# Optimization experiments

Hardware: AMD Instinct MI355X
Metric: run time of the kernel (lower is better)

Reference implementation:

```python
import jax, jax.numpy as jnp
import numpy as np

N = 50000          # total nodes (1000 graphs x 50 agents)
E = 800000         # edges
B = 1000           # batch of graphs -> one agent node each
IN_DIM = 64
HID = 32           # hidden_dim == TransformerConv out_channels per head
HEADS = 4
OUT_DIM = 5
FINAL = HID + HID * HEADS * 2  # 288


def _tconv(x, src, dst, wq, bq, wk, bk, wv, bv):
    """PyG TransformerConv, root_weight=False, concat=True, no edge_attr."""
    n = x.shape[0]
    q = (x @ wq + bq).reshape(n, HEADS, HID)
    k = (x @ wk + bk).reshape(n, HEADS, HID)
    v = (x @ wv + bv).reshape(n, HEADS, HID)
    # per-edge attention logits: query at target, key at source
    alpha = jnp.sum(q[dst] * k[src], axis=-1) / jnp.sqrt(jnp.float32(HID))  # [E, HEADS]
    # segment softmax over incoming edges of each target node
    amax = jax.lax.stop_gradient(jax.ops.segment_max(alpha, dst, num_segments=n))
    ex = jnp.exp(alpha - amax[dst])
    denom = jax.ops.segment_sum(ex, dst, num_segments=n)
    attn = ex / (denom[dst] + 1e-16)                                        # [E, HEADS]
    out = jax.ops.segment_sum(v[src] * attn[..., None], dst, num_segments=n)
    return out.reshape(n, HEADS * HID)


def setup_inputs() -> dict:
    key = jax.random.key(0)
    ks = jax.random.split(key, 24)
    g = lambda i, shape, fan: (jax.random.normal(ks[i], shape, jnp.float32)
                               / jnp.sqrt(jnp.float32(fan)))
    d1 = HID * HEADS  # conv1 output width / conv2 input width
    inp = {
        "x": jax.random.normal(ks[0], (N, IN_DIM), jnp.float32),
        "edge_index": jax.random.randint(ks[1], (2, E), 0, N, jnp.int64),
        "dm_mask": (jax.random.uniform(ks[2], (N, 1)) > 0.5).astype(jnp.float32),
        "global_indices": jax.random.randint(ks[3], (B,), 0, N, jnp.int64),
        # encoder MLP: in -> hid (relu) -> hid
        "enc_w1": g(4, (IN_DIM, HID), IN_DIM), "enc_b1": jnp.zeros((HID,), jnp.float32),
        "enc_w2": g(5, (HID, HID), HID),       "enc_b2": jnp.zeros((HID,), jnp.float32),
        # conv1: hid -> heads*hid
        "c1_wq": g(6, (HID, d1), HID), "c1_bq": jnp.zeros((d1,), jnp.float32),
        "c1_wk": g(7, (HID, d1), HID), "c1_bk": jnp.zeros((d1,), jnp.float32),
        "c1_wv": g(8, (HID, d1), HID), "c1_bv": jnp.zeros((d1,), jnp.float32),
        # conv2: heads*hid -> heads*hid
        "c2_wq": g(9, (d1, d1), d1),  "c2_bq": jnp.zeros((d1,), jnp.float32),
        "c2_wk": g(10, (d1, d1), d1), "c2_bk": jnp.zeros((d1,), jnp.float32),
        "c2_wv": g(11, (d1, d1), d1), "c2_bv": jnp.zeros((d1,), jnp.float32),
        # output head
        "out_w": g(12, (FINAL, OUT_DIM), FINAL),
        "out_b": jnp.zeros((OUT_DIM,), jnp.float32),
    }
    return inp


def reference(x, edge_index, dm_mask, global_indices,
              enc_w1, enc_b1, enc_w2, enc_b2,
              c1_wq, c1_bq, c1_wk, c1_bk, c1_wv, c1_bv,
              c2_wq, c2_bq, c2_wk, c2_bk, c2_wv, c2_bv,
              out_w, out_b):
    src, dst = edge_index[0], edge_index[1]
    # encoder MLP + relu (forward applies F.relu on encoder output)
    h = jax.nn.relu(x @ enc_w1 + enc_b1)
    h = jax.nn.relu(h @ enc_w2 + enc_b2)            # [N, HID]
    x1 = h[global_indices]                          # [B, HID]
    h = jax.nn.relu(_tconv(h, src, dst, c1_wq, c1_bq, c1_wk, c1_bk, c1_wv, c1_bv))
    x2 = h[global_indices]                          # [B, HEADS*HID]
    h = h * dm_mask                                 # decision-maker masking
    h = jax.nn.relu(_tconv(h, src, dst, c2_wq, c2_bq, c2_wk, c2_bk, c2_wv, c2_bv))
    x3 = h[global_indices]                          # [B, HEADS*HID]
    x_cat = jnp.concatenate([x1, x2, x3], axis=1)   # [B, FINAL]
    return x_cat @ out_w + out_b                    # [B, OUT_DIM]
```

## Files before the change

### kernel.cpp

```cpp
#include <hip/hip_runtime.h>
#include <math.h>


typedef _Float16 half8 __attribute__((ext_vector_type(8)));
typedef float f32x4 __attribute__((ext_vector_type(4)));

#define CAP 64
#define ECHUNK 8192

__device__ inline half8 h8zero() {
    half8 r;
#pragma unroll
    for (int j = 0; j < 8; ++j) r[j] = (_Float16)0.f;
    return r;
}

__device__ __forceinline__ void enc_body(const float* __restrict__ x,
                                         const float* __restrict__ w1, const float* __restrict__ b1,
                                         const float* __restrict__ w2, const float* __restrict__ b2,
                                         _Float16* __restrict__ h0, int n, int bn,
                                         float* __restrict__ smem) {
    float* W1s = smem;
    float* W2s = smem + 2048;
    float* B1s = smem + 3072;
    float* B2s = smem + 3104;
    float* xs  = smem + 3136;
    float* hs  = smem + 3648;
    int t = threadIdx.x;
    for (int i = t; i < 64 * 32; i += 256) W1s[i] = w1[i];
    for (int i = t; i < 32 * 32; i += 256) W2s[i] = w2[i];
    if (t < 32) { B1s[t] = b1[t]; B2s[t] = b2[t]; }
    if (t < 128) {
        int row = t >> 4;
        float4 val = make_float4(0.f, 0.f, 0.f, 0.f);
        if (bn + row < n) val = *(const float4*)(x + (size_t)bn * 64 + t * 4);
        ((float4*)xs)[t] = val;
    }
    __syncthreads();
    int nn = t >> 5, c = t & 31;
    float acc = B1s[c];
#pragma unroll
    for (int i = 0; i < 64; ++i) acc += xs[nn * 64 + i] * W1s[i * 32 + c];
    acc = fmaxf(acc, 0.f);
    hs[nn * 32 + c] = acc;
    __syncthreads();
    float acc2 = B2s[c];
#pragma unroll
    for (int i = 0; i < 32; ++i) acc2 += hs[nn * 32 + i] * W2s[i * 32 + c];
    acc2 = fmaxf(acc2, 0.f);
    int node = bn + nn;
    if (node < n) h0[(size_t)node * 32 + c] = (_Float16)acc2;
}

__global__ __launch_bounds__(256)
void prep_kernel(const float* __restrict__ x,
                 const float* __restrict__ ew1, const float* __restrict__ eb1,
                 const float* __restrict__ ew2, const float* __restrict__ eb2,
                 _Float16* __restrict__ h0,
                 const float* __restrict__ q1, const float* __restrict__ k1,
                 const float* __restrict__ v1, _Float16* __restrict__ WT1,
                 const float* __restrict__ q2, const float* __restrict__ k2,
                 const float* __restrict__ v2, _Float16* __restrict__ WT2,
                 const int* __restrict__ srcv, const int* __restrict__ dstv,
                 int* __restrict__ deg, int* __restrict__ colb,
                 int n, int e, int edgeb, int wtb) {
    __shared__ float smem[3904];
    int b = blockIdx.x, t = threadIdx.x;
    if (b < edgeb) {
        int g  = b & 7;
        int ci = b >> 3;
        int npg = (n + 7) / 8;
        int lo = g * npg;
        int hi = lo + npg; if (hi > n) hi = n;
        int e0 = ci * ECHUNK;
        int e1 = e0 + ECHUNK; if (e1 > e) e1 = e;
        for (int i = e0 + t * 4; i < e1; i += 1024) {
            if (i + 3 < e1) {
                int4 dv = *(const int4*)(dstv + i);
                int4 sv = *(const int4*)(srcv + i);
#pragma unroll
                for (int j = 0; j < 4; ++j) {
                    int d = (&dv.x)[j];
                    if (d >= lo && d < hi) {
                        int slot = atomicAdd(&deg[d], 1);
                        if (slot < CAP) colb[d * CAP + slot] = (&sv.x)[j];
                    }
                }
            } else {
                for (int i2 = i; i2 < e1; ++i2) {
                    int d = dstv[i2];
                    if (d >= lo && d < hi) {
                        int slot = atomicAdd(&deg[d], 1);
                        if (slot < CAP) colb[d * CAP + slot] = srcv[i2];
                    }
                }
            }
        }
    } else if (b < edgeb + wtb) {
        int tid = (b - edgeb) * 256 + t;
        const int n1 = 3 * 128 * 32;
        if (tid < n1) {
            int z = tid / (128 * 32);
            int rem = tid % (128 * 32);
            int c = rem / 32, k = rem % 32;
            const float* w = (z == 0) ? q1 : ((z == 1) ? k1 : v1);
            WT1[tid] = (_Float16)w[k * 128 + c];
        } else {
            int i = tid - n1;
            if (i < 3 * 128 * 128) {
                int z = i / (128 * 128);
                int rem = i % (128 * 128);
                int c = rem / 128, k = rem % 128;
                const float* w = (z == 0) ? q2 : ((z == 1) ? k2 : v2);
                WT2[i] = (_Float16)w[k * 128 + c];
            }
        }
    } else {
        enc_body(x, ew1, eb1, ew2, eb2, h0, n, (b - edgeb - wtb) * 8, smem);
    }
}

__device__ __forceinline__ void qkv_body(const _Float16* __restrict__ X, const float* __restrict__ mask,
                                         const _Float16* __restrict__ WT,
                                         const float* __restrict__ Bq, const float* __restrict__ Bk,
                                         const float* __restrict__ Bv,
                                         _Float16* __restrict__ Q, _Float16* __restrict__ KV,
                                         int n, int IN, int bx, int z,
                                         _Float16* __restrict__ Xs, _Float16* __restrict__ Ws) {
    int t = threadIdx.x;
    int bm = bx * 64;
    const float* Bz = (z == 0) ? Bq : ((z == 1) ? Bk : Bv);
    _Float16* Y;
    size_t ystride;
    if (z == 0) { Y = Q; ystride = 128; }
    else        { Y = KV + (z == 1 ? 0 : 128); ystride = 256; }

    int lane = t & 63, w = t >> 6;
    int wr = w >> 1, wc = w & 1;
    int fr = lane & 15, k0 = (lane >> 4) * 8;
    f32x4 acc[2][4];
#pragma unroll
    for (int i = 0; i < 2; ++i)
#pragma unroll
        for (int j = 0; j < 4; ++j)
#pragma unroll
            for (int r = 0; r < 4; ++r) acc[i][j][r] = 0.f;

    int srow = t >> 2, sseg = (t & 3) * 8;
    int snode = bm + srow;
    const _Float16* xbase = X + (size_t)snode * IN + sseg;
    const _Float16* wbase = WT + (size_t)(z * 128) * IN + sseg;
    bool xvalid = (snode < n);
    if (xvalid && mask) xvalid = (mask[snode] != 0.f);

    for (int kt = 0; kt < IN; kt += 32) {
        half8 xv = h8zero();
        if (xvalid) xv = *(const half8*)(xbase + kt);
        half8 wv0 = *(const half8*)(wbase + (size_t)srow * IN + kt);
        half8 wv1 = *(const half8*)(wbase + (size_t)(64 + srow) * IN + kt);
        __syncthreads();
        *(half8*)&Xs[srow * 40 + sseg] = xv;
        *(half8*)&Ws[srow * 40 + sseg] = wv0;
        *(half8*)&Ws[(64 + srow) * 40 + sseg] = wv1;
        __syncthreads();
        half8 a0 = *(const half8*)&Xs[(wr * 32 + fr) * 40 + k0];
        half8 a1 = *(const half8*)&Xs[(wr * 32 + 16 + fr) * 40 + k0];
#pragma unroll
        for (int tc = 0; tc < 4; ++tc) {
            half8 bfr = *(const half8*)&Ws[(wc * 64 + tc * 16 + fr) * 40 + k0];
            acc[0][tc] = __builtin_amdgcn_mfma_f32_16x16x32_f16(a0, bfr, acc[0][tc], 0, 0, 0);
            acc[1][tc] = __builtin_amdgcn_mfma_f32_16x16x32_f16(a1, bfr, acc[1][tc], 0, 0, 0);
        }
    }
#pragma unroll
    for (int tc = 0; tc < 4; ++tc) {
        int colc = wc * 64 + tc * 16 + fr;
        float bias = Bz[colc];
#pragma unroll
        for (int tr = 0; tr < 2; ++tr) {
#pragma unroll
            for (int reg = 0; reg < 4; ++reg) {
                int node = bm + wr * 32 + tr * 16 + (lane >> 4) * 4 + reg;
                if (node < n) Y[(size_t)node * ystride + colc] = (_Float16)(acc[tr][tc][reg] + bias);
            }
        }
    }
}

__global__ __launch_bounds__(256)
void qkv_kernel(const _Float16* __restrict__ X, const float* __restrict__ mask,
                const _Float16* __restrict__ WT,
                const float* __restrict__ Bq, const float* __restrict__ Bk,
                const float* __restrict__ Bv,
                _Float16* __restrict__ Q, _Float16* __restrict__ KV, int n, int IN) {
    __shared__ _Float16 Xs[64 * 40];
    __shared__ _Float16 Ws[128 * 40];
    qkv_body(X, mask, WT, Bq, Bk, Bv, Q, KV, n, IN, blockIdx.x, blockIdx.y, Xs, Ws);
}

__global__ __launch_bounds__(256)
void attn_kernel(const _Float16* __restrict__ q, const _Float16* __restrict__ kv,
                 const int* __restrict__ deg, const int* __restrict__ col,
                 _Float16* __restrict__ out, int n) {
    int w = threadIdx.x >> 6;
    int lane = threadIdx.x & 63;
    int node = blockIdx.x * 4 + w;
    if (node >= n) return;
    int es = lane >> 4;
    int l = lane & 15;
    int d0 = l * 8;
    float qf[8];
    {
        half8 qh = *(const half8*)(q + (size_t)node * 128 + d0);
#pragma unroll
        for (int j = 0; j < 8; ++j) qf[j] = (float)qh[j];
    }
    int start = node * CAP;
    int len = deg[node];
    len = (len > CAP) ? CAP : len;
    float s = 0.f;
    float acc[8];
#pragma unroll
    for (int j = 0; j < 8; ++j) acc[j] = 0.f;
    const float sc = 0.17677669529663689f * 1.4426950408889634f;

    for (int i = es; i < len; i += 4) {
        int srcn = col[start + i];
        const _Float16* row = kv + (size_t)srcn * 256 + d0;
        half8 kf = *(const half8*)row;
        float dot = 0.f;
#pragma unroll
        for (int j = 0; j < 8; ++j) dot += qf[j] * (float)kf[j];
        dot += __shfl_xor(dot, 1);
        dot += __shfl_xor(dot, 2);
        float a = fminf(fmaxf(dot * sc, -120.f), 120.f);
        float p = __builtin_amdgcn_exp2f(a);
        half8 vf = *(const half8*)(row + 128);
        s += p;
#pragma unroll
        for (int j = 0; j < 8; ++j) acc[j] += p * (float)vf[j];
    }
#pragma unroll
    for (int half = 16; half <= 32; half <<= 1) {
        s += __shfl_xor(s, half);
#pragma unroll
        for (int j = 0; j < 8; ++j) acc[j] += __shfl_xor(acc[j], half);
    }
    if (es == 0) {
        float inv = 1.f / (s + 1e-16f);
        half8 r;
#pragma unroll
        for (int j = 0; j < 8; ++j) r[j] = (_Float16)fmaxf(acc[j] * inv, 0.f);
        *(half8*)(out + (size_t)node * 128 + d0) = r;
    }
}

__global__ void head_kernel(const _Float16* __restrict__ h0, const _Float16* __restrict__ h1,
                            const _Float16* __restrict__ h2, const int* __restrict__ gi,
                            const float* __restrict__ ow, const float* __restrict__ ob,
                            float* __restrict__ out, int bsz) {
    int idx = blockIdx.x * 256 + threadIdx.x;
    if (idx >= bsz * 5) return;
    int b = idx / 5, c = idx % 5;
    int g = gi[b];
    float acc = ob[c];
    const _Float16* r0 = h0 + (size_t)g * 32;
#pragma unroll
    for (int i = 0; i < 32; ++i) acc += (float)r0[i] * ow[i * 5 + c];
    const _Float16* r1 = h1 + (size_t)g * 128;
#pragma unroll
    for (int i = 0; i < 128; ++i) acc += (float)r1[i] * ow[(32 + i) * 5 + c];
    const _Float16* r2 = h2 + (size_t)g * 128;
#pragma unroll
    for (int i = 0; i < 128; ++i) acc += (float)r2[i] * ow[(160 + i) * 5 + c];
    out[idx] = acc;
}

extern "C" void kernel_launch(void* const* d_in, const int* in_sizes, int n_in,
                              void* d_out, int out_size, void* d_ws, size_t ws_size,
                              hipStream_t stream) {
    const float* x    = (const float*)d_in[0];
    const int*   ei   = (const int*)d_in[1];
    const float* dm   = (const float*)d_in[2];
    const int*   gi   = (const int*)d_in[3];
    const float* ew1  = (const float*)d_in[4];
    const float* eb1  = (const float*)d_in[5];
    const float* ew2  = (const float*)d_in[6];
    const float* eb2  = (const float*)d_in[7];
    const float* c1wq = (const float*)d_in[8];
    const float* c1bq = (const float*)d_in[9];
    const float* c1wk = (const float*)d_in[10];
    const float* c1bk = (const float*)d_in[11];
    const float* c1wv = (const float*)d_in[12];
    const float* c1bv = (const float*)d_in[13];
    const float* c2wq = (const float*)d_in[14];
    const float* c2bq = (const float*)d_in[15];
    const float* c2wk = (const float*)d_in[16];
    const float* c2bk = (const float*)d_in[17];
    const float* c2wv = (const float*)d_in[18];
    const float* c2bv = (const float*)d_in[19];
    const float* ow   = (const float*)d_in[20];
    const float* ob   = (const float*)d_in[21];
    float* out = (float*)d_out;

    int N = in_sizes[0] / 64;
    int E = in_sizes[1] / 2;
    int B = in_sizes[3];
    const int* srcv = ei;
    const int* dstv = ei + E;

    char* ws = (char*)d_ws;
    size_t off = 0;
    auto alloc = [&](size_t bytes) -> void* {
        void* p = ws + off;
        off += (bytes + 255) & ~(size_t)255;
        return p;
    };
    _Float16* h0   = (_Float16*)alloc((size_t)N * 32 * 2);
    _Float16* h1   = (_Float16*)alloc((size_t)N * 128 * 2);
    _Float16* h2   = (_Float16*)alloc((size_t)N * 128 * 2);
    _Float16* Q    = (_Float16*)alloc((size_t)N * 128 * 2);
    _Float16* KV   = (_Float16*)alloc((size_t)N * 256 * 2);
    _Float16* WT1  = (_Float16*)alloc((size_t)3 * 128 * 32 * 2);
    _Float16* WT2  = (_Float16*)alloc((size_t)3 * 128 * 128 * 2);
    int* deg   = (int*)alloc((size_t)N * 4);
    int* colb  = (int*)alloc((size_t)N * CAP * 4);

    hipMemsetAsync(deg, 0, (size_t)N * 4, stream);

    int edgeb = ((E + ECHUNK - 1) / ECHUNK) * 8;
    int encb  = (N + 7) / 8;
    int nqx   = (N + 63) / 64;
    int wtb   = (3 * 128 * 32 + 3 * 128 * 128 + 255) / 256;

    prep_kernel<<<edgeb + wtb + encb, 256, 0, stream>>>(
        x, ew1, eb1, ew2, eb2, h0,
        c1wq, c1wk, c1wv, WT1, c2wq, c2wk, c2wv, WT2,
        srcv, dstv, deg, colb, N, E, edgeb, wtb);

    dim3 gq(nqx, 3);
    qkv_kernel<<<gq, 256, 0, stream>>>(h0, nullptr, WT1, c1bq, c1bk, c1bv, Q, KV, N, 32);
    attn_kernel<<<(N + 3) / 4, 256, 0, stream>>>(Q, KV, deg, colb, h1, N);
    qkv_kernel<<<gq, 256, 0, stream>>>(h1, dm, WT2, c2bq, c2bk, c2bv, Q, KV, N, 128);
    attn_kernel<<<(N + 3) / 4, 256, 0, stream>>>(Q, KV, deg, colb, h2, N);

    head_kernel<<<(B * 5 + 255) / 256, 256, 0, stream>>>(h0, h1, h2, gi, ow, ob, out, B);
}
```

Baseline: 217.5 us.

## Move edge bucketing into first QKV launch and fold deg zeroing into init

Drops the hipMemsetAsync by zeroing the degree array inside the first (init) kernel, which also runs the weight transpose and encoder. The edge-bucketing blocks move out of that kernel into a new mid kernel that also runs the first-layer QKV projection. This removes one launch and one memset, and lets the atomic-heavy edge scatter run alongside the QKV GEMM instead of alongside the encoder. The cost is a heterogeneous grid where the slow atomic blocks may dominate the tail.

Measured after the change: 216.7 us (median of 2 runs). Within noise of the previous version (-0.4%).

```diff
diff --git a/kernel.cpp b/kernel.cpp
--- a/kernel.cpp
+++ b/kernel.cpp
@@ -53,7 +53,7 @@
 }
 
 __global__ __launch_bounds__(256)
-void prep_kernel(const float* __restrict__ x,
+void init_kernel(const float* __restrict__ x,
                  const float* __restrict__ ew1, const float* __restrict__ eb1,
                  const float* __restrict__ ew2, const float* __restrict__ eb2,
                  _Float16* __restrict__ h0,
@@ -61,43 +61,15 @@
                  const float* __restrict__ v1, _Float16* __restrict__ WT1,
                  const float* __restrict__ q2, const float* __restrict__ k2,
                  const float* __restrict__ v2, _Float16* __restrict__ WT2,
-                 const int* __restrict__ srcv, const int* __restrict__ dstv,
-                 int* __restrict__ deg, int* __restrict__ colb,
-                 int n, int e, int edgeb, int wtb) {
+                 int* __restrict__ deg,
+                 int n, int zb, int wtb) {
     __shared__ float smem[3904];
     int b = blockIdx.x, t = threadIdx.x;
-    if (b < edgeb) {
-        int g  = b & 7;
-        int ci = b >> 3;
-        int npg = (n + 7) / 8;
-        int lo = g * npg;
-        int hi = lo + npg; if (hi > n) hi = n;
-        int e0 = ci * ECHUNK;
-        int e1 = e0 + ECHUNK; if (e1 > e) e1 = e;
-        for (int i = e0 + t * 4; i < e1; i += 1024) {
-            if (i + 3 < e1) {
-                int4 dv = *(const int4*)(dstv + i);
-                int4 sv = *(const int4*)(srcv + i);
-#pragma unroll
-                for (int j = 0; j < 4; ++j) {
-                    int d = (&dv.x)[j];
-                    if (d >= lo && d < hi) {
-                        int slot = atomicAdd(&deg[d], 1);
-                        if (slot < CAP) colb[d * CAP + slot] = (&sv.x)[j];
-                    }
-                }
-            } else {
-                for (int i2 = i; i2 < e1; ++i2) {
-                    int d = dstv[i2];
-                    if (d >= lo && d < hi) {
-                        int slot = atomicAdd(&deg[d], 1);
-                        if (slot < CAP) colb[d * CAP + slot] = srcv[i2];
-                    }
-                }
-            }
-        }
-    } else if (b < edgeb + wtb) {
-        int tid = (b - edgeb) * 256 + t;
+    if (b < zb) {
+        int i = b * 256 + t;
+        if (i < n) deg[i] = 0;
+    } else if (b < zb + wtb) {
+        int tid = (b - zb) * 256 + t;
         const int n1 = 3 * 128 * 32;
         if (tid < n1) {
             int z = tid / (128 * 32);
@@ -116,7 +88,7 @@
             }
         }
     } else {
-        enc_body(x, ew1, eb1, ew2, eb2, h0, n, (b - edgeb - wtb) * 8, smem);
+        enc_body(x, ew1, eb1, ew2, eb2, h0, n, (b - zb - wtb) * 8, smem);
     }
 }
 
@@ -184,6 +156,53 @@
                 if (node < n) Y[(size_t)node * ystride + colc] = (_Float16)(acc[tr][tc][reg] + bias);
             }
         }
+    }
+}
+
+__global__ __launch_bounds__(256)
+void mid_kernel(const int* __restrict__ srcv, const int* __restrict__ dstv,
+                int* __restrict__ deg, int* __restrict__ colb,
+                const _Float16* __restrict__ h0, const _Float16* __restrict__ WT1,
+                const float* __restrict__ bq, const float* __restrict__ bk,
+                const float* __restrict__ bv,
+                _Float16* __restrict__ Q, _Float16* __restrict__ KV,
+                int n, int e, int edgeb, int nqx) {
+    __shared__ _Float16 sm[64 * 40 + 128 * 40];
+    int b = blockIdx.x, t = threadIdx.x;
+    if (b < edgeb) {
+        int g  = b & 7;
+        int ci = b >> 3;
+        int npg = (n + 7) / 8;
+        int lo = g * npg;
+        int hi = lo + npg; if (hi > n) hi = n;
+        int e0 = ci * ECHUNK;
+        int e1 = e0 + ECHUNK; if (e1 > e) e1 = e;
+        for (int i = e0 + t * 4; i < e1; i += 1024) {
+            if (i + 3 < e1) {
+                int4 dv = *(const int4*)(dstv + i);
+                int4 sv = *(const int4*)(srcv + i);
+#pragma unroll
+                for (int j = 0; j < 4; ++j) {
+                    int d = (&dv.x)[j];
+                    if (d >= lo && d < hi) {
+                        int slot = atomicAdd(&deg[d], 1);
+                        if (slot < CAP) colb[d * CAP + slot] = (&sv.x)[j];
+                    }
+                }
+            } else {
+                for (int i2 = i; i2 < e1; ++i2) {
+                    int d = dstv[i2];
+                    if (d >= lo && d < hi) {
+                        int slot = atomicAdd(&deg[d], 1);
+                        if (slot < CAP) colb[d * CAP + slot] = srcv[i2];
+                    }
+                }
+            }
+        }
+    } else {
+        int r = b - edgeb;
+        qkv_body(h0, nullptr, WT1, bq, bk, bv, Q, KV, n, 32, r % nqx, r / nqx,
+                 sm, sm + 64 * 40);
     }
 }
 
@@ -326,21 +345,23 @@
     int* deg   = (int*)alloc((size_t)N * 4);
     int* colb  = (int*)alloc((size_t)N * CAP * 4);
 
-    hipMemsetAsync(deg, 0, (size_t)N * 4, stream);
-
+    int zb    = (N + 255) / 256;
     int edgeb = ((E + ECHUNK - 1) / ECHUNK) * 8;
     int encb  = (N + 7) / 8;
     int nqx   = (N + 63) / 64;
     int wtb   = (3 * 128 * 32 + 3 * 128 * 128 + 255) / 256;
 
-    prep_kernel<<<edgeb + wtb + encb, 256, 0, stream>>>(
+    init_kernel<<<zb + wtb + encb, 256, 0, stream>>>(
         x, ew1, eb1, ew2, eb2, h0,
         c1wq, c1wk, c1wv, WT1, c2wq, c2wk, c2wv, WT2,
-        srcv, dstv, deg, colb, N, E, edgeb, wtb);
+        deg, N, zb, wtb);
+
+    mid_kernel<<<edgeb + 3 * nqx, 256, 0, stream>>>(
+        srcv, dstv, deg, colb, h0, WT1, c1bq, c1bk, c1bv, Q, KV, N, E, edgeb, nqx);
+
+    attn_kernel<<<(N + 3) / 4, 256, 0, stream>>>(Q, KV, deg, colb, h1, N);
 
     dim3 gq(nqx, 3);
-    qkv_kernel<<<gq, 256, 0, stream>>>(h0, nullptr, WT1, c1bq, c1bk, c1bv, Q, KV, N, 32);
-    attn_kernel<<<(N + 3) / 4, 256, 0, stream>>>(Q, KV, deg, colb, h1, N);
     qkv_kernel<<<gq, 256, 0, stream>>>(h1, dm, WT2, c2bq, c2bk, c2bv, Q, KV, N, 128);
     attn_kernel<<<(N + 3) / 4, 256, 0, stream>>>(Q, KV, deg, colb, h2, N);
 
```
